# Kernel tuning notes

Hardware: AMD Instinct MI355X
Metric: run time of the kernel (lower is better)

## Reference

```python
import jax, jax.numpy as jnp
import numpy as np


def setup_inputs() -> dict:
    key = jax.random.key(0)
    ks = jax.random.split(key, 9)
    B, Q, K, F, C = 16, 2048, 2048, 128, 2
    q = jax.random.normal(ks[0], (B, Q, F), dtype=jnp.float32)
    k = jax.random.normal(ks[1], (B, K, F), dtype=jnp.float32)
    v = jax.random.normal(ks[2], (B, K, F), dtype=jnp.float32)
    coords_q = jax.random.uniform(ks[3], (B, Q, C), dtype=jnp.float32)
    coords_k = jax.random.uniform(ks[4], (B, K, C), dtype=jnp.float32)
    attn_mask = jax.random.randint(ks[5], (B, Q, K), 0, 2).astype(jnp.bool_)
    alibi_mask = jax.random.randint(ks[6], (B, Q, K), 0, 2).astype(jnp.bool_)
    bias_scale = jax.random.uniform(ks[7], (1,), dtype=jnp.float32)  # nn.Parameter(torch.rand(1))
    running_mean = jnp.ones((1,), dtype=jnp.float32)  # RunningMeanScaler buffer (eval mode)
    return {"q": q, "k": k, "v": v, "coords_q": coords_q, "coords_k": coords_k,
            "attn_mask": attn_mask, "alibi_mask": alibi_mask,
            "bias_scale": bias_scale, "running_mean": running_mean}


def reference(q, k, v, coords_q, coords_k, attn_mask, alibi_mask, bias_scale, running_mean):
    # [b,q,k] attention logits
    scale = jnp.asarray(k.shape[-1], q.dtype) ** -0.5
    weight_logits = jnp.einsum('bqf,bkf->bqk', q, k) * scale
    # pairwise coordinate distances [b,q,k]
    diff = coords_q[:, :, None, :] - coords_k[:, None, :, :]
    distances = jnp.sqrt(jnp.sum(diff * diff, axis=-1))
    scaled_distances = (distances / running_mean) * bias_scale  # broadcast scalars
    masked_distances = jnp.where(alibi_mask, jnp.zeros((), distances.dtype), scaled_distances)
    weights = jax.nn.softmax(weight_logits, axis=-1)
    masked = jnp.where(attn_mask, jnp.zeros((), weights.dtype), weights - masked_distances)
    attention = jnp.einsum('bqk,bkf->bqf', masked, v)
    return attention
```

## Files before the change

### kernel.cpp

```cpp
#include <hip/hip_runtime.h>
#include <stdint.h>

#define B_  16
#define QL  2048
#define KL  2048
#define FD  128
#define BQ  64
#define BK  32
#define NSTEP (KL/BK)

#define KSTR  136
#define VTOFF 4352
#define BUFS  8448
#define PSTR  40
#define MSTR  36

typedef __attribute__((ext_vector_type(8))) short bf16x8;
typedef __attribute__((ext_vector_type(4))) float f32x4;
typedef __attribute__((ext_vector_type(4))) int   i32x4;

__device__ __forceinline__ unsigned short f2b(float f) {
  union { float f; unsigned u; } x; x.f = f;
  return (unsigned short)((x.u + 0x8000u) >> 16);
}

__global__ __launch_bounds__(256, 2) void alibi_attn(
    const float* __restrict__ qp,
    const float* __restrict__ kp,
    const float* __restrict__ vp,
    const float* __restrict__ cqp,
    const float* __restrict__ ckp,
    const int* __restrict__ amp,
    const int* __restrict__ almp,
    const float* __restrict__ bsp,
    const float* __restrict__ rmp,
    float* __restrict__ outp)
{
  __shared__ unsigned short kv[2 * BUFS];
  __shared__ unsigned short plds[4][2][16 * PSTR];
  __shared__ unsigned char  mlds[2][64 * MSTR];

  const int t    = threadIdx.x;
  const int w    = t >> 6;
  const int lane = t & 63;
  const int l15  = lane & 15;
  const int q4   = lane >> 4;

  const int bid  = blockIdx.x;
  const int xcd  = bid & 7, slot = bid >> 3;
  const int b    = (xcd << 1) | (slot >> 5);
  const int qbase = (slot & 31) * BQ;

  const float bscale = bsp[0] / rmp[0];
  const float sl2 = 0.08838834764831845f * 1.44269504089f;

  const int kr_st = t >> 3, fb_st = (t & 7) * 4;
  const int vrq = t >> 5, vfc = t & 31;
  const int vwp = ((vrq ^ ((vfc >> 1) & 7)) * 4);
  const int vwa = VTOFF + vfc * 32 + vwp;
  const int mrow = t >> 2, mcol = (t & 3) * 8;
  const long long mgbase = ((long long)(b * QL + qbase + mrow)) * KL + mcol;
  const int mlo = mrow * MSTR + mcol;
  const int sv_r = l15 >> 1;
  const int voff0 = ((2 * q4) ^ sv_r) * 4;
  const int voff1 = ((2 * q4 + 1) ^ sv_r) * 4;
  const int vrb = VTOFF + l15 * 32;

  {
    const float* qg = qp + ((long long)(b * QL + qbase)) * FD;
    #pragma unroll
    for (int i = 0; i < 8; ++i) {
      int idx = t + 256 * i;
      float4 u = ((const float4*)qg)[idx];
      int row = idx >> 5, col = (idx & 31) * 4;
      ushort4 s4; s4.x = f2b(u.x); s4.y = f2b(u.y); s4.z = f2b(u.z); s4.w = f2b(u.w);
      *(ushort4*)&kv[row * KSTR + col] = s4;
    }
  }
  __syncthreads();
  bf16x8 qfrag[4];
  {
    const int m = w * 16 + l15;
    #pragma unroll
    for (int fs = 0; fs < 4; ++fs)
      qfrag[fs] = *(const bf16x8*)&kv[m * KSTR + fs * 32 + q4 * 8];
  }
  float cqx[4], cqy[4];
  #pragma unroll
  for (int r = 0; r < 4; ++r) {
    const int qg_ = qbase + w * 16 + q4 * 4 + r;
    float2 c2 = *(const float2*)(cqp + ((long long)(b * QL + qg_)) * 2);
    cqx[r] = c2.x; cqy[r] = c2.y;
  }
  __syncthreads();

  const float* kgb = kp + ((long long)b * KL) * FD;
  const float* vgb = vp + ((long long)b * KL) * FD;

  float ckx_b[2][2], cky_b[2][2];

  {
    i32x4 a0 = __builtin_nontemporal_load((const i32x4*)(amp + mgbase));
    i32x4 a1 = __builtin_nontemporal_load((const i32x4*)(amp + mgbase + 4));
    i32x4 g0 = __builtin_nontemporal_load((const i32x4*)(almp + mgbase));
    i32x4 g1 = __builtin_nontemporal_load((const i32x4*)(almp + mgbase + 4));
    float4 kld[4];
    float  vsc[4][4];
    #pragma unroll
    for (int i = 0; i < 4; ++i)
      kld[i] = *(const float4*)(kgb + (long long)kr_st * FD + fb_st + 32 * i);
    #pragma unroll
    for (int d = 0; d < 4; ++d)
      #pragma unroll
      for (int kk = 0; kk < 4; ++kk)
        vsc[d][kk] = vgb[(long long)(4 * vrq + kk) * FD + vfc + 32 * d];
    #pragma unroll
    for (int s = 0; s < 2; ++s) {
      float2 c2 = *(const float2*)(ckp + ((long long)(b * KL + s * 16 + l15)) * 2);
      ckx_b[0][s] = c2.x; cky_b[0][s] = c2.y;
    }
    unsigned ua = (unsigned)(a0[0] | (a0[1] << 8) | (a0[2] << 16) | (a0[3] << 24));
    unsigned ul = (unsigned)(g0[0] | (g0[1] << 8) | (g0[2] << 16) | (g0[3] << 24));
    *(unsigned*)&mlds[0][mlo] = ua | (ul << 1);
    ua = (unsigned)(a1[0] | (a1[1] << 8) | (a1[2] << 16) | (a1[3] << 24));
    ul = (unsigned)(g1[0] | (g1[1] << 8) | (g1[2] << 16) | (g1[3] << 24));
    *(unsigned*)&mlds[0][mlo + 4] = ua | (ul << 1);
    #pragma unroll
    for (int i = 0; i < 4; ++i) {
      ushort4 s4; s4.x = f2b(kld[i].x); s4.y = f2b(kld[i].y);
      s4.z = f2b(kld[i].z); s4.w = f2b(kld[i].w);
      *(ushort4*)&kv[kr_st * KSTR + fb_st + 32 * i] = s4;
    }
    #pragma unroll
    for (int d = 0; d < 4; ++d) {
      short4 w4;
      w4.x = (short)f2b(vsc[d][0]); w4.y = (short)f2b(vsc[d][1]);
      w4.z = (short)f2b(vsc[d][2]); w4.w = (short)f2b(vsc[d][3]);
      *(short4*)&kv[vwa + 1024 * d] = w4;
    }
  }
  __syncthreads();

  f32x4 O1[8], O2[8];
  #pragma unroll
  for (int n = 0; n < 8; ++n) {
    O1[n] = (f32x4){0.f, 0.f, 0.f, 0.f};
    O2[n] = (f32x4){0.f, 0.f, 0.f, 0.f};
  }
  float lsum[4] = {0.f, 0.f, 0.f, 0.f};

  #pragma unroll 2
  for (int kt = 0; kt < NSTEP; ++kt) {
    const int cur = kt & 1, nxt = cur ^ 1;
    const unsigned short* kb = kv + cur * BUFS;
    unsigned short*       nb = kv + nxt * BUFS;
    const int ktp = (kt + 1 < NSTEP) ? (kt + 1) : kt;
    const int k0p = ktp * BK;

    i32x4 a0 = __builtin_nontemporal_load((const i32x4*)(amp + mgbase + k0p));
    i32x4 a1 = __builtin_nontemporal_load((const i32x4*)(amp + mgbase + k0p + 4));
    i32x4 g0 = __builtin_nontemporal_load((const i32x4*)(almp + mgbase + k0p));
    i32x4 g1 = __builtin_nontemporal_load((const i32x4*)(almp + mgbase + k0p + 4));
    float4 kld[4];
    float  vsc[4][4];
    #pragma unroll
    for (int i = 0; i < 4; ++i)
      kld[i] = *(const float4*)(kgb + (long long)(k0p + kr_st) * FD + fb_st + 32 * i);
    #pragma unroll
    for (int d = 0; d < 4; ++d)
      #pragma unroll
      for (int kk = 0; kk < 4; ++kk)
        vsc[d][kk] = vgb[(long long)(k0p + 4 * vrq + kk) * FD + vfc + 32 * d];
    #pragma unroll
    for (int s = 0; s < 2; ++s) {
      float2 c2 = *(const float2*)(ckp + ((long long)(b * KL + k0p + s * 16 + l15)) * 2);
      ckx_b[nxt][s] = c2.x; cky_b[nxt][s] = c2.y;
    }

    f32x4 S0 = (f32x4){0.f, 0.f, 0.f, 0.f};
    f32x4 S1 = (f32x4){0.f, 0.f, 0.f, 0.f};
    #pragma unroll
    for (int fs = 0; fs < 4; ++fs) {
      bf16x8 kb0 = *(const bf16x8*)&kb[(l15)      * KSTR + fs * 32 + q4 * 8];
      bf16x8 kb1 = *(const bf16x8*)&kb[(16 + l15) * KSTR + fs * 32 + q4 * 8];
      S0 = __builtin_amdgcn_mfma_f32_16x16x32_bf16(qfrag[fs], kb0, S0, 0, 0, 0);
      S1 = __builtin_amdgcn_mfma_f32_16x16x32_bf16(qfrag[fs], kb1, S1, 0, 0, 0);
    }

    #pragma unroll
    for (int s = 0; s < 2; ++s) {
      const f32x4 Sv = s ? S1 : S0;
      #pragma unroll
      for (int r = 0; r < 4; ++r) {
        unsigned char m = mlds[cur][(w * 16 + q4 * 4 + r) * MSTR + s * 16 + l15];
        float e = __builtin_amdgcn_exp2f(Sv[r] * sl2);
        lsum[r] += e;
        float dx = cqx[r] - ckx_b[cur][s], dy = cqy[r] - cky_b[cur][s];
        float d  = sqrtf(fmaf(dx, dx, dy * dy)) * bscale;
        float wv = (m & 1) ? 0.f : e;
        float tv = m ? 0.f : d;
        const int mm = q4 * 4 + r, c = s * 16 + l15;
        plds[w][0][mm * PSTR + c] = f2b(wv);
        plds[w][1][mm * PSTR + c] = f2b(tv);
      }
    }

    bf16x8 aw = *(const bf16x8*)&plds[w][0][l15 * PSTR + q4 * 8];
    bf16x8 at = *(const bf16x8*)&plds[w][1][l15 * PSTR + q4 * 8];
    #pragma unroll
    for (int n = 0; n < 8; ++n) {
      short4 v0 = *(const short4*)&kb[vrb + 512 * n + voff0];
      short4 v1 = *(const short4*)&kb[vrb + 512 * n + voff1];
      bf16x8 vb;
      vb[0] = v0.x; vb[1] = v0.y; vb[2] = v0.z; vb[3] = v0.w;
      vb[4] = v1.x; vb[5] = v1.y; vb[6] = v1.z; vb[7] = v1.w;
      O1[n] = __builtin_amdgcn_mfma_f32_16x16x32_bf16(aw, vb, O1[n], 0, 0, 0);
      O2[n] = __builtin_amdgcn_mfma_f32_16x16x32_bf16(at, vb, O2[n], 0, 0, 0);
    }

    unsigned ua = (unsigned)(a0[0] | (a0[1] << 8) | (a0[2] << 16) | (a0[3] << 24));
    unsigned ul = (unsigned)(g0[0] | (g0[1] << 8) | (g0[2] << 16) | (g0[3] << 24));
    *(unsigned*)&mlds[nxt][mlo] = ua | (ul << 1);
    ua = (unsigned)(a1[0] | (a1[1] << 8) | (a1[2] << 16) | (a1[3] << 24));
    ul = (unsigned)(g1[0] | (g1[1] << 8) | (g1[2] << 16) | (g1[3] << 24));
    *(unsigned*)&mlds[nxt][mlo + 4] = ua | (ul << 1);
    #pragma unroll
    for (int i = 0; i < 4; ++i) {
      ushort4 s4; s4.x = f2b(kld[i].x); s4.y = f2b(kld[i].y);
      s4.z = f2b(kld[i].z); s4.w = f2b(kld[i].w);
      *(ushort4*)&nb[kr_st * KSTR + fb_st + 32 * i] = s4;
    }
    #pragma unroll
    for (int d = 0; d < 4; ++d) {
      short4 w4;
      w4.x = (short)f2b(vsc[d][0]); w4.y = (short)f2b(vsc[d][1]);
      w4.z = (short)f2b(vsc[d][2]); w4.w = (short)f2b(vsc[d][3]);
      *(short4*)&nb[vwa + 1024 * d] = w4;
    }
    __syncthreads();
  }

  #pragma unroll
  for (int off = 1; off < 16; off <<= 1) {
    #pragma unroll
    for (int r = 0; r < 4; ++r) lsum[r] += __shfl_xor(lsum[r], off, 64);
  }
  float linv[4];
  #pragma unroll
  for (int r = 0; r < 4; ++r) linv[r] = 1.0f / lsum[r];

  #pragma unroll
  for (int n = 0; n < 8; ++n) {
    #pragma unroll
    for (int r = 0; r < 4; ++r) {
      const int qg_ = qbase + w * 16 + q4 * 4 + r;
      const int f   = n * 16 + l15;
      float val = O1[n][r] * linv[r] - O2[n][r];
      __builtin_nontemporal_store(val, outp + ((long long)(b * QL + qg_)) * FD + f);
    }
  }
}

extern "C" void kernel_launch(void* const* d_in, const int* in_sizes, int n_in,
                              void* d_out, int out_size, void* d_ws, size_t ws_size,
                              hipStream_t stream) {
  const float* q   = (const float*)d_in[0];
  const float* k   = (const float*)d_in[1];
  const float* v   = (const float*)d_in[2];
  const float* cq  = (const float*)d_in[3];
  const float* ck  = (const float*)d_in[4];
  const int*   am  = (const int*)d_in[5];
  const int*   alm = (const int*)d_in[6];
  const float* bs  = (const float*)d_in[7];
  const float* rm  = (const float*)d_in[8];
  float*       out = (float*)d_out;

  dim3 grid(B_ * (QL / BQ));
  dim3 block(256);
  hipLaunchKernelGGL(alibi_attn, grid, block, 0, stream,
                     q, k, v, cq, ck, am, alm, bs, rm, out);
}
```

Before: 731.5 us.

## Pre-convert K and transposed V to bf16 in workspace before attention kernel

Adds two pre-pass kernels: one converts K to bf16 and one converts V to bf16 while transposing it into per-tile, feature-major blocks, both written to the workspace. The main kernel then loads bf16 K and V with wide 16-byte loads and copies them straight into LDS with no per-tile conversion, and the V-operand reads become single 16-byte LDS loads. Each of the 32 query blocks per batch previously re-read fp32 K/V and redid the conversion, so this halves global K/V traffic and removes repeated conversion ALU work. The cost is two extra launches and a pass over K and V to write the workspace.

```diff
diff --git a/kernel.cpp b/kernel.cpp
--- a/kernel.cpp
+++ b/kernel.cpp
@@ -11,9 +11,11 @@
 
 #define KSTR  136
 #define VTOFF 4352
-#define BUFS  8448
+#define VTSTR 36
+#define BUFS  8960
 #define PSTR  40
 #define MSTR  36
+#define WS_HALF (B_*KL*FD)
 
 typedef __attribute__((ext_vector_type(8))) short bf16x8;
 typedef __attribute__((ext_vector_type(4))) float f32x4;
@@ -24,10 +26,39 @@
   return (unsigned short)((x.u + 0x8000u) >> 16);
 }
 
+__global__ __launch_bounds__(256) void conv_k(const float* __restrict__ kp,
+                                              unsigned short* __restrict__ kb) {
+  int idx = (blockIdx.x * 256 + threadIdx.x) * 4;
+  float4 u = *(const float4*)(kp + idx);
+  ushort4 s4; s4.x = f2b(u.x); s4.y = f2b(u.y); s4.z = f2b(u.z); s4.w = f2b(u.w);
+  *(ushort4*)(kb + idx) = s4;
+}
+
+__global__ __launch_bounds__(256) void conv_vt(const float* __restrict__ vp,
+                                               unsigned short* __restrict__ vt) {
+  __shared__ float tl[32 * 132];
+  const int t = threadIdx.x, b = blockIdx.x >> 6, kt = blockIdx.x & 63;
+  const int r = t >> 3, f0 = (t & 7) * 16;
+  const float* src = vp + ((long long)(b * KL + kt * 32 + r)) * FD + f0;
+  #pragma unroll
+  for (int i = 0; i < 4; ++i)
+    *(float4*)&tl[r * 132 + f0 + 4 * i] = *(const float4*)(src + 4 * i);
+  __syncthreads();
+  const int f = t >> 1, half = t & 1;
+  bf16x8 o0, o1;
+  #pragma unroll
+  for (int j = 0; j < 8; ++j)  o0[j] = (short)f2b(tl[(half * 16 + j) * 132 + f]);
+  #pragma unroll
+  for (int j = 0; j < 8; ++j)  o1[j] = (short)f2b(tl[(half * 16 + 8 + j) * 132 + f]);
+  unsigned short* dst = vt + ((long long)((b * 64 + kt) * FD + f)) * 32 + half * 16;
+  *(bf16x8*)dst = o0;
+  *(bf16x8*)(dst + 8) = o1;
+}
+
 __global__ __launch_bounds__(256, 2) void alibi_attn(
+    const unsigned short* __restrict__ kbp,
+    const unsigned short* __restrict__ vtp,
     const float* __restrict__ qp,
-    const float* __restrict__ kp,
-    const float* __restrict__ vp,
     const float* __restrict__ cqp,
     const float* __restrict__ ckp,
     const int* __restrict__ amp,
@@ -54,17 +85,11 @@
   const float bscale = bsp[0] / rmp[0];
   const float sl2 = 0.08838834764831845f * 1.44269504089f;
 
-  const int kr_st = t >> 3, fb_st = (t & 7) * 4;
-  const int vrq = t >> 5, vfc = t & 31;
-  const int vwp = ((vrq ^ ((vfc >> 1) & 7)) * 4);
-  const int vwa = VTOFF + vfc * 32 + vwp;
+  const int kr_st = t >> 3, kc_st = (t & 7) * 16;
+  const int vf_st = t >> 1, vh_st = (t & 1) * 16;
   const int mrow = t >> 2, mcol = (t & 3) * 8;
   const long long mgbase = ((long long)(b * QL + qbase + mrow)) * KL + mcol;
   const int mlo = mrow * MSTR + mcol;
-  const int sv_r = l15 >> 1;
-  const int voff0 = ((2 * q4) ^ sv_r) * 4;
-  const int voff1 = ((2 * q4 + 1) ^ sv_r) * 4;
-  const int vrb = VTOFF + l15 * 32;
 
   {
     const float* qg = qp + ((long long)(b * QL + qbase)) * FD;
@@ -94,8 +119,8 @@
   }
   __syncthreads();
 
-  const float* kgb = kp + ((long long)b * KL) * FD;
-  const float* vgb = vp + ((long long)b * KL) * FD;
+  const unsigned short* kgb = kbp + (long long)b * KL * FD;
+  const unsigned short* vgb = vtp + (long long)b * KL * FD;
 
   float ckx_b[2][2], cky_b[2][2];
 
@@ -104,16 +129,10 @@
     i32x4 a1 = __builtin_nontemporal_load((const i32x4*)(amp + mgbase + 4));
     i32x4 g0 = __builtin_nontemporal_load((const i32x4*)(almp + mgbase));
     i32x4 g1 = __builtin_nontemporal_load((const i32x4*)(almp + mgbase + 4));
-    float4 kld[4];
-    float  vsc[4][4];
-    #pragma unroll
-    for (int i = 0; i < 4; ++i)
-      kld[i] = *(const float4*)(kgb + (long long)kr_st * FD + fb_st + 32 * i);
-    #pragma unroll
-    for (int d = 0; d < 4; ++d)
-      #pragma unroll
-      for (int kk = 0; kk < 4; ++kk)
-        vsc[d][kk] = vgb[(long long)(4 * vrq + kk) * FD + vfc + 32 * d];
+    bf16x8 k0l = *(const bf16x8*)(kgb + kr_st * FD + kc_st);
+    bf16x8 k1l = *(const bf16x8*)(kgb + kr_st * FD + kc_st + 8);
+    bf16x8 v0l = *(const bf16x8*)(vgb + t * 16);
+    bf16x8 v1l = *(const bf16x8*)(vgb + t * 16 + 8);
     #pragma unroll
     for (int s = 0; s < 2; ++s) {
       float2 c2 = *(const float2*)(ckp + ((long long)(b * KL + s * 16 + l15)) * 2);
@@ -125,19 +144,10 @@
     ua = (unsigned)(a1[0] | (a1[1] << 8) | (a1[2] << 16) | (a1[3] << 24));
     ul = (unsigned)(g1[0] | (g1[1] << 8) | (g1[2] << 16) | (g1[3] << 24));
     *(unsigned*)&mlds[0][mlo + 4] = ua | (ul << 1);
-    #pragma unroll
-    for (int i = 0; i < 4; ++i) {
-      ushort4 s4; s4.x = f2b(kld[i].x); s4.y = f2b(kld[i].y);
-      s4.z = f2b(kld[i].z); s4.w = f2b(kld[i].w);
-      *(ushort4*)&kv[kr_st * KSTR + fb_st + 32 * i] = s4;
-    }
-    #pragma unroll
-    for (int d = 0; d < 4; ++d) {
-      short4 w4;
-      w4.x = (short)f2b(vsc[d][0]); w4.y = (short)f2b(vsc[d][1]);
-      w4.z = (short)f2b(vsc[d][2]); w4.w = (short)f2b(vsc[d][3]);
-      *(short4*)&kv[vwa + 1024 * d] = w4;
-    }
+    *(bf16x8*)&kv[kr_st * KSTR + kc_st]     = k0l;
+    *(bf16x8*)&kv[kr_st * KSTR + kc_st + 8] = k1l;
+    *(bf16x8*)&kv[VTOFF + vf_st * VTSTR + vh_st]     = v0l;
+    *(bf16x8*)&kv[VTOFF + vf_st * VTSTR + vh_st + 8] = v1l;
   }
   __syncthreads();
 
@@ -161,16 +171,10 @@
     i32x4 a1 = __builtin_nontemporal_load((const i32x4*)(amp + mgbase + k0p + 4));
     i32x4 g0 = __builtin_nontemporal_load((const i32x4*)(almp + mgbase + k0p));
     i32x4 g1 = __builtin_nontemporal_load((const i32x4*)(almp + mgbase + k0p + 4));
-    float4 kld[4];
-    float  vsc[4][4];
-    #pragma unroll
-    for (int i = 0; i < 4; ++i)
-      kld[i] = *(const float4*)(kgb + (long long)(k0p + kr_st) * FD + fb_st + 32 * i);
-    #pragma unroll
-    for (int d = 0; d < 4; ++d)
-      #pragma unroll
-      for (int kk = 0; kk < 4; ++kk)
-        vsc[d][kk] = vgb[(long long)(k0p + 4 * vrq + kk) * FD + vfc + 32 * d];
+    bf16x8 k0l = *(const bf16x8*)(kgb + (k0p + kr_st) * FD + kc_st);
+    bf16x8 k1l = *(const bf16x8*)(kgb + (k0p + kr_st) * FD + kc_st + 8);
+    bf16x8 v0l = *(const bf16x8*)(vgb + ktp * (32 * FD) + t * 16);
+    bf16x8 v1l = *(const bf16x8*)(vgb + ktp * (32 * FD) + t * 16 + 8);
     #pragma unroll
     for (int s = 0; s < 2; ++s) {
       float2 c2 = *(const float2*)(ckp + ((long long)(b * KL + k0p + s * 16 + l15)) * 2);
@@ -209,11 +213,7 @@
     bf16x8 at = *(const bf16x8*)&plds[w][1][l15 * PSTR + q4 * 8];
     #pragma unroll
     for (int n = 0; n < 8; ++n) {
-      short4 v0 = *(const short4*)&kb[vrb + 512 * n + voff0];
-      short4 v1 = *(const short4*)&kb[vrb + 512 * n + voff1];
-      bf16x8 vb;
-      vb[0] = v0.x; vb[1] = v0.y; vb[2] = v0.z; vb[3] = v0.w;
-      vb[4] = v1.x; vb[5] = v1.y; vb[6] = v1.z; vb[7] = v1.w;
+      bf16x8 vb = *(const bf16x8*)&kb[VTOFF + (n * 16 + l15) * VTSTR + q4 * 8];
       O1[n] = __builtin_amdgcn_mfma_f32_16x16x32_bf16(aw, vb, O1[n], 0, 0, 0);
       O2[n] = __builtin_amdgcn_mfma_f32_16x16x32_bf16(at, vb, O2[n], 0, 0, 0);
     }
@@ -224,19 +224,10 @@
     ua = (unsigned)(a1[0] | (a1[1] << 8) | (a1[2] << 16) | (a1[3] << 24));
     ul = (unsigned)(g1[0] | (g1[1] << 8) | (g1[2] << 16) | (g1[3] << 24));
     *(unsigned*)&mlds[nxt][mlo + 4] = ua | (ul << 1);
-    #pragma unroll
-    for (int i = 0; i < 4; ++i) {
-      ushort4 s4; s4.x = f2b(kld[i].x); s4.y = f2b(kld[i].y);
-      s4.z = f2b(kld[i].z); s4.w = f2b(kld[i].w);
-      *(ushort4*)&nb[kr_st * KSTR + fb_st + 32 * i] = s4;
-    }
-    #pragma unroll
-    for (int d = 0; d < 4; ++d) {
-      short4 w4;
-      w4.x = (short)f2b(vsc[d][0]); w4.y = (short)f2b(vsc[d][1]);
-      w4.z = (short)f2b(vsc[d][2]); w4.w = (short)f2b(vsc[d][3]);
-      *(short4*)&nb[vwa + 1024 * d] = w4;
-    }
+    *(bf16x8*)&nb[kr_st * KSTR + kc_st]     = k0l;
+    *(bf16x8*)&nb[kr_st * KSTR + kc_st + 8] = k1l;
+    *(bf16x8*)&nb[VTOFF + vf_st * VTSTR + vh_st]     = v0l;
+    *(bf16x8*)&nb[VTOFF + vf_st * VTSTR + vh_st + 8] = v1l;
     __syncthreads();
   }
 
@@ -275,8 +266,14 @@
   const float* rm  = (const float*)d_in[8];
   float*       out = (float*)d_out;
 
+  unsigned short* kb = (unsigned short*)d_ws;
+  unsigned short* vt = kb + WS_HALF;
+
+  hipLaunchKernelGGL(conv_k,  dim3(WS_HALF / 1024), dim3(256), 0, stream, k, kb);
+  hipLaunchKernelGGL(conv_vt, dim3(B_ * 64),        dim3(256), 0, stream, v, vt);
+
   dim3 grid(B_ * (QL / BQ));
   dim3 block(256);
   hipLaunchKernelGGL(alibi_attn, grid, block, 0, stream,
-                     q, k, v, cq, ck, am, alm, bs, rm, out);
-}
+                     kb, vt, q, cq, ck, am, alm, bs, rm, out);
+}
```

Result: faster. 665.3 us (-9.0%).
